# Performance work log

Measured on AMD Instinct MI355X. Metric: run time of the kernel, lower is better.

Reference implementation:

```python
import jax, jax.numpy as jnp
import numpy as np

B, N, M, D = 64, 197, 65, 768


def setup_inputs() -> dict:
    key = jax.random.key(0)
    k1, k2, k3 = jax.random.split(key, 3)
    image = jax.random.normal(k1, (B, N, D), dtype=jnp.float32)
    text = jax.random.normal(k2, (B, M, D), dtype=jnp.float32)
    pm = jax.random.randint(k3, (B, M), 0, 2).astype(jnp.int32)
    pm = pm.at[:, :2].set(0)  # CLS + first real token always valid
    logit_scale = jnp.ones((), dtype=jnp.float32)
    return {"image": image, "text": text, "padding_masks": pm, "logit_scale": logit_scale}


def _ce_with_diag_labels(logits):
    # F.cross_entropy(logits, arange(B)): mean of -log_softmax diag
    return -jnp.mean(jnp.diagonal(jax.nn.log_softmax(logits, axis=-1)))


def reference(image, text, padding_masks, logit_scale):
    # include_cls_token=False: original computes full [B,B,N,M] then slices
    # [:, :, 1:, 1:]; we compute the sliced tokens directly (same math).
    img = image[:, 1:, :]                   # [B, N-1, D]
    txt = text[:, 1:, :]                    # [B, M-1, D]
    pm = padding_masks[:, 1:].astype(bool)  # [B, M-1] True = padded

    # sim[i,j,n,m] = logit_scale * <img_i,n , txt_j,m>
    sim = logit_scale * jnp.einsum('ind,jmd->ijnm', img, txt)  # [B,B,N-1,M-1]

    # Original masks with NaN along mask of batch-row i (broadcast over j,n).
    # logits_per_image: nan_to_num(-inf) -> max over m -> mean over n
    sim_img = jnp.where(pm[:, None, None, :], -jnp.inf, sim)
    logits_per_image = jnp.mean(jnp.max(sim_img, axis=3), axis=2)  # [B,B]

    # logits_per_text: max over n (NaN cols stay NaN) -> nanmean over m.
    # Equivalent masked mean over valid m (mask constant along n).
    max_n = jnp.max(sim, axis=2)                         # [B,B,M-1]
    valid = ~pm                                          # [B,M-1]
    cnt = jnp.sum(valid, axis=1).astype(sim.dtype)       # [B]
    logits_per_text = jnp.sum(
        jnp.where(valid[:, None, :], max_n, 0.0), axis=2
    ) / cnt[:, None]                                     # [B,B]

    loss = 0.5 * (_ce_with_diag_labels(logits_per_image)
                  + _ce_with_diag_labels(logits_per_text))
    targets = jnp.arange(logits_per_image.shape[0], dtype=jnp.int32)
    return loss, logits_per_image, logits_per_text, targets
```

## Files before the change

### kernel.cpp

```cpp
#include <hip/hip_runtime.h>

typedef _Float16 half8 __attribute__((ext_vector_type(8)));
typedef float floatx4 __attribute__((ext_vector_type(4)));
typedef float float4v __attribute__((ext_vector_type(4)));

#define DIM   768
#define NROW  196
#define AUNITS (64 * 13 * 24 * 64)
#define TUNITS (64 * 4 * 24 * 64)
#define A_HALFS ((size_t)AUNITS * 8)
#define BJ_HALFS (24 * 4 * 64 * 8)

__device__ __forceinline__ void gl_lds16(const _Float16* g, _Float16* l) {
  __builtin_amdgcn_global_load_lds(
      (const __attribute__((address_space(1))) unsigned int*)g,
      (__attribute__((address_space(3))) unsigned int*)l, 16, 0, 0);
}

__global__ __launch_bounds__(256) void repack(const float* __restrict__ img,
                                              const float* __restrict__ txt,
                                              _Float16* __restrict__ Apk,
                                              _Float16* __restrict__ Bpk) {
  int gid = blockIdx.x * 256 + threadIdx.x;
  const float* src;
  _Float16* dst;
  if (gid < AUNITS) {
    int l = gid & 63, g = gid >> 6;
    int s = g % 24; g /= 24;
    int tau = g % 13; int i = g / 13;
    int n = tau * 16 + (l & 15); if (n > 195) n = 195;
    src = img + (size_t)i * 197 * 768 + (size_t)(n + 1) * 768 + s * 32 + (l >> 4) * 8;
    dst = Apk + (size_t)gid * 8;
  } else {
    int u = gid - AUNITS;
    int l = u & 63, g = u >> 6;
    int ct = g & 3; g >>= 2;
    int s = g % 24; int j = g / 24;
    int m = ct * 16 + (l & 15);
    src = txt + (size_t)j * 65 * 768 + (size_t)(m + 1) * 768 + s * 32 + (l >> 4) * 8;
    dst = Bpk + (size_t)u * 8;
  }
  float4v v0 = *(const float4v*)src;
  float4v v1 = *(const float4v*)(src + 4);
  half8 h;
  h[0] = (_Float16)v0[0]; h[1] = (_Float16)v0[1]; h[2] = (_Float16)v0[2]; h[3] = (_Float16)v0[3];
  h[4] = (_Float16)v1[0]; h[5] = (_Float16)v1[1]; h[6] = (_Float16)v1[2]; h[7] = (_Float16)v1[3];
  *(half8*)dst = h;
}

__global__ __launch_bounds__(256, 2) void sim_kernel(const _Float16* __restrict__ Apk,
                                                     const _Float16* __restrict__ Bpk,
                                                     const int* __restrict__ pm,
                                                     const float* __restrict__ ls,
                                                     float* __restrict__ lpi,
                                                     float* __restrict__ lpt) {
  __shared__ _Float16 Bsh[32768];

  const int jb = blockIdx.x, i = blockIdx.y;
  const int tid = threadIdx.x;
  const int wave = tid >> 6, lane = tid & 63;
  const int r16 = lane & 15;
  const int lane8 = lane * 8;

  const _Float16* Ai = Apk + (size_t)i * 13 * 24 * 512;
  const _Float16* pA[4];
  pA[0] = Ai + (size_t)(wave)     * 24 * 512 + lane8;
  pA[1] = Ai + (size_t)(wave + 4) * 24 * 512 + lane8;
  pA[2] = Ai + (size_t)(wave + 8) * 24 * 512 + lane8;
  pA[3] = Ai + (size_t)12         * 24 * 512 + lane8;
  const _Float16* Bg = Bpk + (size_t)(2 * jb) * BJ_HALFS;

#pragma unroll
  for (int r8 = 0; r8 < 8; ++r8) {
    int u = wave * 8 + r8;
    int jj = u >> 4, rr = u & 15;
    gl_lds16(Bg + (size_t)jj * BJ_HALFS + rr * 512 + lane8,
             Bsh + jj * 8192 + rr * 512);
  }

  half8 af[2][4];
#pragma unroll
  for (int d = 0; d < 2; ++d)
#pragma unroll
    for (int t = 0; t < 4; ++t)
      af[d][t] = *(const half8*)(pA[t] + d * 512);

  floatx4 acc[2][3][4];
  floatx4 acc12[2];
  acc12[0] = (floatx4){0.f, 0.f, 0.f, 0.f};
  acc12[1] = (floatx4){0.f, 0.f, 0.f, 0.f};
#pragma unroll
  for (int jj = 0; jj < 2; ++jj)
#pragma unroll
    for (int t = 0; t < 3; ++t)
#pragma unroll
      for (int cc = 0; cc < 4; ++cc)
        acc[jj][t][cc] = (floatx4){0.f, 0.f, 0.f, 0.f};

#pragma unroll
  for (int c = 0; c < 6; ++c) {
    __syncthreads();
    if (c < 5) {
#pragma unroll
      for (int r8 = 0; r8 < 8; ++r8) {
        int u = wave * 8 + r8;
        int jj = u >> 4, rr = u & 15;
        gl_lds16(Bg + (size_t)jj * BJ_HALFS + (c + 1) * 8192 + rr * 512 + lane8,
                 Bsh + ((c + 1) & 1) * 16384 + jj * 8192 + rr * 512);
      }
    }
#pragma unroll
    for (int sc = 0; sc < 4; ++sc) {
      const int s = c * 4 + sc;
      const int base = (c & 1) * 16384 + sc * 2048 + lane8;
      half8 b0[4], b1[4];
#pragma unroll
      for (int cc = 0; cc < 4; ++cc) {
        int ct = (wave + cc) & 3;
        b0[cc] = *(const half8*)(Bsh + base + ct * 512);
        b1[cc] = *(const half8*)(Bsh + base + 8192 + ct * 512);
      }
      half8 a0 = af[s & 1][0], a1 = af[s & 1][1], a2 = af[s & 1][2], a3 = af[s & 1][3];
      if (s < 22) {
#pragma unroll
        for (int t = 0; t < 4; ++t) af[s & 1][t] = *(const half8*)(pA[t] + (s + 2) * 512);
      }
#pragma unroll
      for (int cc = 0; cc < 4; ++cc) {
        acc[0][0][cc] = __builtin_amdgcn_mfma_f32_16x16x32_f16(a0, b0[cc], acc[0][0][cc], 0, 0, 0);
        acc[0][1][cc] = __builtin_amdgcn_mfma_f32_16x16x32_f16(a1, b0[cc], acc[0][1][cc], 0, 0, 0);
        acc[0][2][cc] = __builtin_amdgcn_mfma_f32_16x16x32_f16(a2, b0[cc], acc[0][2][cc], 0, 0, 0);
        acc[1][0][cc] = __builtin_amdgcn_mfma_f32_16x16x32_f16(a0, b1[cc], acc[1][0][cc], 0, 0, 0);
        acc[1][1][cc] = __builtin_amdgcn_mfma_f32_16x16x32_f16(a1, b1[cc], acc[1][1][cc], 0, 0, 0);
        acc[1][2][cc] = __builtin_amdgcn_mfma_f32_16x16x32_f16(a2, b1[cc], acc[1][2][cc], 0, 0, 0);
      }
      acc12[0] = __builtin_amdgcn_mfma_f32_16x16x32_f16(a3, b0[0], acc12[0], 0, 0, 0);
      acc12[1] = __builtin_amdgcn_mfma_f32_16x16x32_f16(a3, b1[0], acc12[1], 0, 0, 0);
    }
  }

  const float sgl = ls[0];
  bool msk[4];
  int colc[4];
#pragma unroll
  for (int cc = 0; cc < 4; ++cc) {
    colc[cc] = ((wave + cc) & 3) * 16 + r16;
    msk[cc] = pm[i * 65 + 1 + colc[cc]] != 0;
  }

  float rowsum[2] = {0.f, 0.f};
  float cmv[2][4];
#pragma unroll
  for (int jj = 0; jj < 2; ++jj) {
#pragma unroll
    for (int t = 0; t < 3; ++t) {
#pragma unroll
      for (int r = 0; r < 4; ++r) {
        float rm = -__builtin_inff();
#pragma unroll
        for (int cc = 0; cc < 4; ++cc) {
          float v = acc[jj][t][cc][r] * sgl;
          rm = fmaxf(rm, msk[cc] ? -__builtin_inff() : v);
        }
#pragma unroll
        for (int off = 1; off < 16; off <<= 1)
          rm = fmaxf(rm, __shfl_xor(rm, off, 64));
        rowsum[jj] += rm;
      }
    }
#pragma unroll
    for (int off = 1; off < 64; off <<= 1) rowsum[jj] += __shfl_xor(rowsum[jj], off, 64);

#pragma unroll
    for (int cc = 0; cc < 4; ++cc) {
      float cm = -__builtin_inff();
#pragma unroll
      for (int t = 0; t < 3; ++t)
#pragma unroll
        for (int r = 0; r < 4; ++r)
          cm = fmaxf(cm, acc[jj][t][cc][r] * sgl);
      cm = fmaxf(cm, __shfl_xor(cm, 16, 64));
      cm = fmaxf(cm, __shfl_xor(cm, 32, 64));
      cmv[jj][cc] = cm;
    }
  }

  __syncthreads();
  float* colmaxS = (float*)Bsh;
  float* t12S    = (float*)Bsh + 512;
  float* wsumS   = (float*)Bsh + 1024;

  if (lane == 0) { wsumS[wave] = rowsum[0]; wsumS[4 + wave] = rowsum[1]; }
  if (lane < 16) {
#pragma unroll
    for (int jj = 0; jj < 2; ++jj) {
#pragma unroll
      for (int cc = 0; cc < 4; ++cc) colmaxS[jj * 256 + wave * 64 + colc[cc]] = cmv[jj][cc];
#pragma unroll
      for (int r = 0; r < 4; ++r) t12S[jj * 256 + r * 64 + wave * 16 + r16] = acc12[jj][r] * sgl;
    }
  }
  __syncthreads();

  if (tid < 128) {
    const int jj = wave;
    const int col = lane;
    bool valid = pm[i * 65 + 1 + col] == 0;
    const float* cm = colmaxS + jj * 256;
    const float* t12 = t12S + jj * 256;
    float t0 = t12[col], t1 = t12[64 + col], t2 = t12[128 + col], t3 = t12[192 + col];
    float v = fmaxf(fmaxf(cm[col], cm[64 + col]), fmaxf(cm[128 + col], cm[192 + col]));
    v = fmaxf(v, fmaxf(fmaxf(t0, t1), fmaxf(t2, t3)));
    float contrib = valid ? v : 0.f;
    float cntv = valid ? 1.f : 0.f;
    float rs0 = valid ? t0 : -__builtin_inff();
    float rs1 = valid ? t1 : -__builtin_inff();
    float rs2 = valid ? t2 : -__builtin_inff();
    float rs3 = valid ? t3 : -__builtin_inff();
#pragma unroll
    for (int off = 1; off < 64; off <<= 1) {
      contrib += __shfl_xor(contrib, off, 64);
      cntv += __shfl_xor(cntv, off, 64);
      rs0 = fmaxf(rs0, __shfl_xor(rs0, off, 64));
      rs1 = fmaxf(rs1, __shfl_xor(rs1, off, 64));
      rs2 = fmaxf(rs2, __shfl_xor(rs2, off, 64));
      rs3 = fmaxf(rs3, __shfl_xor(rs3, off, 64));
    }
    if (lane == 0) {
      int jout = 2 * jb + jj;
      lpt[i * 64 + jout] = contrib / cntv;
      float wtot = wsumS[jj * 4 + 0] + wsumS[jj * 4 + 1] + wsumS[jj * 4 + 2] + wsumS[jj * 4 + 3];
      lpi[i * 64 + jout] = (wtot * 0.0625f + rs0 + rs1 + rs2 + rs3) / 196.f;
    }
  }
}

__global__ __launch_bounds__(64) void ce_kernel(float* __restrict__ out) {
  const int t = threadIdx.x;
  const float* lpi = out + 1;
  const float* lpt = out + 1 + 4096;

  float mx = -__builtin_inff();
  for (int jj = 0; jj < 64; ++jj) mx = fmaxf(mx, lpi[t * 64 + jj]);
  float se = 0.f;
  for (int jj = 0; jj < 64; ++jj) se += __expf(lpi[t * 64 + jj] - mx);
  float ci = (mx + __logf(se)) - lpi[t * 64 + t];

  float mx2 = -__builtin_inff();
  for (int jj = 0; jj < 64; ++jj) mx2 = fmaxf(mx2, lpt[t * 64 + jj]);
  float se2 = 0.f;
  for (int jj = 0; jj < 64; ++jj) se2 += __expf(lpt[t * 64 + jj] - mx2);
  float ct_ = (mx2 + __logf(se2)) - lpt[t * 64 + t];

  float v = ci + ct_;
#pragma unroll
  for (int off = 1; off < 64; off <<= 1) v += __shfl_xor(v, off, 64);
  if (t == 0) out[0] = 0.5f * v / 64.f;
  out[1 + 8192 + t] = (float)t;
}

extern "C" void kernel_launch(void* const* d_in, const int* in_sizes, int n_in,
                              void* d_out, int out_size, void* d_ws, size_t ws_size,
                              hipStream_t stream) {
  const float* image = (const float*)d_in[0];
  const float* text  = (const float*)d_in[1];
  const int*   pm    = (const int*)d_in[2];
  const float* ls    = (const float*)d_in[3];
  float* out = (float*)d_out;

  _Float16* Apk = (_Float16*)d_ws;
  _Float16* Bpk = Apk + A_HALFS;

  repack<<<(AUNITS + TUNITS) / 256, 256, 0, stream>>>(image, text, Apk, Bpk);

  dim3 grid(32, 64);
  sim_kernel<<<grid, 256, 0, stream>>>(Apk, Bpk, pm, ls, out + 1, out + 1 + 4096);
  ce_kernel<<<1, 64, 0, stream>>>(out);
}
```

Before: 188.2 us.

## Split sim kernel work across eight waves per block instead of four

The similarity kernel moves from 256 to 512 threads per block. Waves 0-4 each own two 16-row image tiles and waves 5-7 own one, replacing the old scheme where each wave held three tiles plus a shared partial-tile path. The special handling for tile 12 (acc12, t12S) is removed and padded rows are now masked in the epilogue by a row < NROW check. This aims to raise occupancy and lower per-wave register pressure, at the cost of uneven work across waves and a doubled LDS reduction footprint.

```diff
diff --git a/kernel.cpp b/kernel.cpp
--- a/kernel.cpp
+++ b/kernel.cpp
@@ -48,7 +48,7 @@
   *(half8*)dst = h;
 }
 
-__global__ __launch_bounds__(256, 2) void sim_kernel(const _Float16* __restrict__ Apk,
+__global__ __launch_bounds__(512, 4) void sim_kernel(const _Float16* __restrict__ Apk,
                                                      const _Float16* __restrict__ Bpk,
                                                      const int* __restrict__ pm,
                                                      const float* __restrict__ ls,
@@ -59,40 +59,36 @@
   const int jb = blockIdx.x, i = blockIdx.y;
   const int tid = threadIdx.x;
   const int wave = tid >> 6, lane = tid & 63;
-  const int r16 = lane & 15;
+  const int quad = lane >> 4, r16 = lane & 15;
   const int lane8 = lane * 8;
+  const int NT = (wave < 5) ? 2 : 1;
+  const int tau0 = wave, tau1 = (wave < 5) ? wave + 8 : wave;
 
   const _Float16* Ai = Apk + (size_t)i * 13 * 24 * 512;
-  const _Float16* pA[4];
-  pA[0] = Ai + (size_t)(wave)     * 24 * 512 + lane8;
-  pA[1] = Ai + (size_t)(wave + 4) * 24 * 512 + lane8;
-  pA[2] = Ai + (size_t)(wave + 8) * 24 * 512 + lane8;
-  pA[3] = Ai + (size_t)12         * 24 * 512 + lane8;
+  const _Float16* pA0 = Ai + (size_t)tau0 * 24 * 512 + lane8;
+  const _Float16* pA1 = Ai + (size_t)tau1 * 24 * 512 + lane8;
   const _Float16* Bg = Bpk + (size_t)(2 * jb) * BJ_HALFS;
 
 #pragma unroll
-  for (int r8 = 0; r8 < 8; ++r8) {
-    int u = wave * 8 + r8;
-    int jj = u >> 4, rr = u & 15;
-    gl_lds16(Bg + (size_t)jj * BJ_HALFS + rr * 512 + lane8,
-             Bsh + jj * 8192 + rr * 512);
-  }
-
-  half8 af[2][4];
-#pragma unroll
-  for (int d = 0; d < 2; ++d)
-#pragma unroll
-    for (int t = 0; t < 4; ++t)
-      af[d][t] = *(const half8*)(pA[t] + d * 512);
-
-  floatx4 acc[2][3][4];
-  floatx4 acc12[2];
-  acc12[0] = (floatx4){0.f, 0.f, 0.f, 0.f};
-  acc12[1] = (floatx4){0.f, 0.f, 0.f, 0.f};
+  for (int r = 0; r < 4; ++r) {
+    int u = wave * 4 + r;
+    int jj = u >> 4, v = u & 15;
+    gl_lds16(Bg + (size_t)jj * BJ_HALFS + v * 512 + lane8,
+             Bsh + jj * 8192 + v * 512);
+  }
+
+  half8 af[2][2];
+#pragma unroll
+  for (int d = 0; d < 2; ++d) {
+    af[d][0] = *(const half8*)(pA0 + d * 512);
+    if (wave < 5) af[d][1] = *(const half8*)(pA1 + d * 512);
+  }
+
+  floatx4 acc[2][2][4];
 #pragma unroll
   for (int jj = 0; jj < 2; ++jj)
 #pragma unroll
-    for (int t = 0; t < 3; ++t)
+    for (int t = 0; t < 2; ++t)
 #pragma unroll
       for (int cc = 0; cc < 4; ++cc)
         acc[jj][t][cc] = (floatx4){0.f, 0.f, 0.f, 0.f};
@@ -102,70 +98,64 @@
     __syncthreads();
     if (c < 5) {
 #pragma unroll
-      for (int r8 = 0; r8 < 8; ++r8) {
-        int u = wave * 8 + r8;
-        int jj = u >> 4, rr = u & 15;
-        gl_lds16(Bg + (size_t)jj * BJ_HALFS + (c + 1) * 8192 + rr * 512 + lane8,
-                 Bsh + ((c + 1) & 1) * 16384 + jj * 8192 + rr * 512);
+      for (int r = 0; r < 4; ++r) {
+        int u = wave * 4 + r;
+        int jj = u >> 4, v = u & 15;
+        gl_lds16(Bg + (size_t)jj * BJ_HALFS + (c + 1) * 8192 + v * 512 + lane8,
+                 Bsh + ((c + 1) & 1) * 16384 + jj * 8192 + v * 512);
       }
     }
 #pragma unroll
     for (int sc = 0; sc < 4; ++sc) {
       const int s = c * 4 + sc;
       const int base = (c & 1) * 16384 + sc * 2048 + lane8;
-      half8 b0[4], b1[4];
+      half8 a0 = af[s & 1][0], a1 = af[s & 1][1];
+      if (s < 22) {
+        af[s & 1][0] = *(const half8*)(pA0 + (s + 2) * 512);
+        if (wave < 5) af[s & 1][1] = *(const half8*)(pA1 + (s + 2) * 512);
+      }
 #pragma unroll
       for (int cc = 0; cc < 4; ++cc) {
-        int ct = (wave + cc) & 3;
-        b0[cc] = *(const half8*)(Bsh + base + ct * 512);
-        b1[cc] = *(const half8*)(Bsh + base + 8192 + ct * 512);
-      }
-      half8 a0 = af[s & 1][0], a1 = af[s & 1][1], a2 = af[s & 1][2], a3 = af[s & 1][3];
-      if (s < 22) {
-#pragma unroll
-        for (int t = 0; t < 4; ++t) af[s & 1][t] = *(const half8*)(pA[t] + (s + 2) * 512);
-      }
-#pragma unroll
-      for (int cc = 0; cc < 4; ++cc) {
-        acc[0][0][cc] = __builtin_amdgcn_mfma_f32_16x16x32_f16(a0, b0[cc], acc[0][0][cc], 0, 0, 0);
-        acc[0][1][cc] = __builtin_amdgcn_mfma_f32_16x16x32_f16(a1, b0[cc], acc[0][1][cc], 0, 0, 0);
-        acc[0][2][cc] = __builtin_amdgcn_mfma_f32_16x16x32_f16(a2, b0[cc], acc[0][2][cc], 0, 0, 0);
-        acc[1][0][cc] = __builtin_amdgcn_mfma_f32_16x16x32_f16(a0, b1[cc], acc[1][0][cc], 0, 0, 0);
-        acc[1][1][cc] = __builtin_amdgcn_mfma_f32_16x16x32_f16(a1, b1[cc], acc[1][1][cc], 0, 0, 0);
-        acc[1][2][cc] = __builtin_amdgcn_mfma_f32_16x16x32_f16(a2, b1[cc], acc[1][2][cc], 0, 0, 0);
-      }
-      acc12[0] = __builtin_amdgcn_mfma_f32_16x16x32_f16(a3, b0[0], acc12[0], 0, 0, 0);
-      acc12[1] = __builtin_amdgcn_mfma_f32_16x16x32_f16(a3, b1[0], acc12[1], 0, 0, 0);
+        half8 b0 = *(const half8*)(Bsh + base + cc * 512);
+        half8 b1 = *(const half8*)(Bsh + base + 8192 + cc * 512);
+        acc[0][0][cc] = __builtin_amdgcn_mfma_f32_16x16x32_f16(a0, b0, acc[0][0][cc], 0, 0, 0);
+        acc[1][0][cc] = __builtin_amdgcn_mfma_f32_16x16x32_f16(a0, b1, acc[1][0][cc], 0, 0, 0);
+        if (wave < 5) {
+          acc[0][1][cc] = __builtin_amdgcn_mfma_f32_16x16x32_f16(a1, b0, acc[0][1][cc], 0, 0, 0);
+          acc[1][1][cc] = __builtin_amdgcn_mfma_f32_16x16x32_f16(a1, b1, acc[1][1][cc], 0, 0, 0);
+        }
+      }
     }
   }
 
   const float sgl = ls[0];
   bool msk[4];
-  int colc[4];
-#pragma unroll
-  for (int cc = 0; cc < 4; ++cc) {
-    colc[cc] = ((wave + cc) & 3) * 16 + r16;
-    msk[cc] = pm[i * 65 + 1 + colc[cc]] != 0;
-  }
+#pragma unroll
+  for (int cc = 0; cc < 4; ++cc)
+    msk[cc] = pm[i * 65 + 1 + cc * 16 + r16] != 0;
 
   float rowsum[2] = {0.f, 0.f};
   float cmv[2][4];
 #pragma unroll
   for (int jj = 0; jj < 2; ++jj) {
 #pragma unroll
-    for (int t = 0; t < 3; ++t) {
-#pragma unroll
-      for (int r = 0; r < 4; ++r) {
-        float rm = -__builtin_inff();
-#pragma unroll
-        for (int cc = 0; cc < 4; ++cc) {
-          float v = acc[jj][t][cc][r] * sgl;
-          rm = fmaxf(rm, msk[cc] ? -__builtin_inff() : v);
+    for (int t = 0; t < 2; ++t) {
+      if (t < NT) {
+        int tau = t ? tau1 : tau0;
+#pragma unroll
+        for (int r = 0; r < 4; ++r) {
+          int row = tau * 16 + quad * 4 + r;
+          float rm = -__builtin_inff();
+#pragma unroll
+          for (int cc = 0; cc < 4; ++cc) {
+            float v = acc[jj][t][cc][r] * sgl;
+            rm = fmaxf(rm, msk[cc] ? -__builtin_inff() : v);
+          }
+#pragma unroll
+          for (int off = 1; off < 16; off <<= 1)
+            rm = fmaxf(rm, __shfl_xor(rm, off, 64));
+          if (row < NROW) rowsum[jj] += rm;
         }
-#pragma unroll
-        for (int off = 1; off < 16; off <<= 1)
-          rm = fmaxf(rm, __shfl_xor(rm, off, 64));
-        rowsum[jj] += rm;
       }
     }
 #pragma unroll
@@ -175,10 +165,16 @@
     for (int cc = 0; cc < 4; ++cc) {
       float cm = -__builtin_inff();
 #pragma unroll
-      for (int t = 0; t < 3; ++t)
-#pragma unroll
-        for (int r = 0; r < 4; ++r)
-          cm = fmaxf(cm, acc[jj][t][cc][r] * sgl);
+      for (int t = 0; t < 2; ++t) {
+        if (t < NT) {
+          int tau = t ? tau1 : tau0;
+#pragma unroll
+          for (int r = 0; r < 4; ++r) {
+            int row = tau * 16 + quad * 4 + r;
+            if (row < NROW) cm = fmaxf(cm, acc[jj][t][cc][r] * sgl);
+          }
+        }
+      }
       cm = fmaxf(cm, __shfl_xor(cm, 16, 64));
       cm = fmaxf(cm, __shfl_xor(cm, 32, 64));
       cmv[jj][cc] = cm;
@@ -187,18 +183,15 @@
 
   __syncthreads();
   float* colmaxS = (float*)Bsh;
-  float* t12S    = (float*)Bsh + 512;
   float* wsumS   = (float*)Bsh + 1024;
 
-  if (lane == 0) { wsumS[wave] = rowsum[0]; wsumS[4 + wave] = rowsum[1]; }
+  if (lane == 0) { wsumS[wave] = rowsum[0]; wsumS[8 + wave] = rowsum[1]; }
   if (lane < 16) {
 #pragma unroll
-    for (int jj = 0; jj < 2; ++jj) {
-#pragma unroll
-      for (int cc = 0; cc < 4; ++cc) colmaxS[jj * 256 + wave * 64 + colc[cc]] = cmv[jj][cc];
-#pragma unroll
-      for (int r = 0; r < 4; ++r) t12S[jj * 256 + r * 64 + wave * 16 + r16] = acc12[jj][r] * sgl;
-    }
+    for (int jj = 0; jj < 2; ++jj)
+#pragma unroll
+      for (int cc = 0; cc < 4; ++cc)
+        colmaxS[jj * 512 + wave * 64 + cc * 16 + r16] = cmv[jj][cc];
   }
   __syncthreads();
 
@@ -206,31 +199,23 @@
     const int jj = wave;
     const int col = lane;
     bool valid = pm[i * 65 + 1 + col] == 0;
-    const float* cm = colmaxS + jj * 256;
-    const float* t12 = t12S + jj * 256;
-    float t0 = t12[col], t1 = t12[64 + col], t2 = t12[128 + col], t3 = t12[192 + col];
-    float v = fmaxf(fmaxf(cm[col], cm[64 + col]), fmaxf(cm[128 + col], cm[192 + col]));
-    v = fmaxf(v, fmaxf(fmaxf(t0, t1), fmaxf(t2, t3)));
+    float v = -__builtin_inff();
+#pragma unroll
+    for (int w = 0; w < 8; ++w) v = fmaxf(v, colmaxS[jj * 512 + w * 64 + col]);
     float contrib = valid ? v : 0.f;
     float cntv = valid ? 1.f : 0.f;
-    float rs0 = valid ? t0 : -__builtin_inff();
-    float rs1 = valid ? t1 : -__builtin_inff();
-    float rs2 = valid ? t2 : -__builtin_inff();
-    float rs3 = valid ? t3 : -__builtin_inff();
 #pragma unroll
     for (int off = 1; off < 64; off <<= 1) {
       contrib += __shfl_xor(contrib, off, 64);
       cntv += __shfl_xor(cntv, off, 64);
-      rs0 = fmaxf(rs0, __shfl_xor(rs0, off, 64));
-      rs1 = fmaxf(rs1, __shfl_xor(rs1, off, 64));
-      rs2 = fmaxf(rs2, __shfl_xor(rs2, off, 64));
-      rs3 = fmaxf(rs3, __shfl_xor(rs3, off, 64));
     }
     if (lane == 0) {
       int jout = 2 * jb + jj;
       lpt[i * 64 + jout] = contrib / cntv;
-      float wtot = wsumS[jj * 4 + 0] + wsumS[jj * 4 + 1] + wsumS[jj * 4 + 2] + wsumS[jj * 4 + 3];
-      lpi[i * 64 + jout] = (wtot * 0.0625f + rs0 + rs1 + rs2 + rs3) / 196.f;
+      float wtot = 0.f;
+#pragma unroll
+      for (int w = 0; w < 8; ++w) wtot += wsumS[jj * 8 + w];
+      lpi[i * 64 + jout] = (wtot * 0.0625f) / 196.f;
     }
   }
 }
@@ -274,6 +259,6 @@
   repack<<<(AUNITS + TUNITS) / 256, 256, 0, stream>>>(image, text, Apk, Bpk);
 
   dim3 grid(32, 64);
-  sim_kernel<<<grid, 256, 0, stream>>>(Apk, Bpk, pm, ls, out + 1, out + 1 + 4096);
+  sim_kernel<<<grid, 512, 0, stream>>>(Apk, Bpk, pm, ls, out + 1, out + 1 + 4096);
   ce_kernel<<<1, 64, 0, stream>>>(out);
 }
```

After: 225.8 us. 20.0% more time.
